# Optimization experiments

Hardware: AMD Instinct MI355X
Metric: run time of the kernel (lower is better)

## Reference

```python
import jax, jax.numpy as jnp
import numpy as np

N_NODES = 50000
NEG_SLOPE = 0.2


def gat_conv(x, src, dst, W, att_src, att_dst, bias, concat):
    # x: [N, F_in], W: [H*D, F_in], att_*: [H, D], bias: [H*D] or [D]
    N = x.shape[0]
    H, D = att_src.shape
    h = (x @ W.T).reshape(N, H, D)                      # [N, H, D]
    a_src = jnp.einsum('nhd,hd->nh', h, att_src)        # [N, H]
    a_dst = jnp.einsum('nhd,hd->nh', h, att_dst)        # [N, H]
    e = jax.nn.leaky_relu(a_src[src] + a_dst[dst], NEG_SLOPE)  # [E, H]
    # softmax over incoming edges of each destination node
    m = jax.ops.segment_max(e, dst, num_segments=N)     # [N, H]
    ex = jnp.exp(e - m[dst])
    denom = jax.ops.segment_sum(ex, dst, num_segments=N)
    alpha = ex / denom[dst]                             # [E, H]
    msg = alpha[:, :, None] * h[src]                    # [E, H, D]
    out = jax.ops.segment_sum(msg, dst, num_segments=N) # [N, H, D]
    out = out.reshape(N, H * D) if concat else out.mean(axis=1)
    return out + bias


def setup_inputs() -> dict:
    key = jax.random.key(0)
    ks = jax.random.split(key, 10)
    nfeat, nhid, nclass, heads = 256, 128, 40, 4
    d1 = nhid // heads  # 32
    E = 800000
    x = jax.random.normal(ks[0], (N_NODES, nfeat), dtype=jnp.float32)
    edge_index = jax.random.randint(ks[1], (2, E), 0, N_NODES, dtype=jnp.int64)
    s = 0.1
    W1 = jax.random.normal(ks[2], (heads * d1, nfeat), dtype=jnp.float32) * s
    att_src1 = jax.random.normal(ks[3], (heads, d1), dtype=jnp.float32) * s
    att_dst1 = jax.random.normal(ks[4], (heads, d1), dtype=jnp.float32) * s
    b1 = jnp.zeros((heads * d1,), dtype=jnp.float32)
    W2 = jax.random.normal(ks[5], (nclass, nhid), dtype=jnp.float32) * s
    att_src2 = jax.random.normal(ks[6], (1, nclass), dtype=jnp.float32) * s
    att_dst2 = jax.random.normal(ks[7], (1, nclass), dtype=jnp.float32) * s
    b2 = jnp.zeros((nclass,), dtype=jnp.float32)
    return {"x": x, "edge_index": edge_index, "W1": W1, "att_src1": att_src1,
            "att_dst1": att_dst1, "b1": b1, "W2": W2, "att_src2": att_src2,
            "att_dst2": att_dst2, "b2": b2}


def reference(x, edge_index, W1, att_src1, att_dst1, b1, W2, att_src2, att_dst2, b2):
    # PyG GATConv adds self-loops by default
    loops = jnp.arange(N_NODES, dtype=edge_index.dtype)
    src = jnp.concatenate([edge_index[0], loops])
    dst = jnp.concatenate([edge_index[1], loops])
    h = gat_conv(x, src, dst, W1, att_src1, att_dst1, b1, concat=True)
    h = jax.nn.relu(h)
    # dropout is identity in eval mode
    out = gat_conv(h, src, dst, W2, att_src2, att_dst2, b2, concat=True)
    return out
```

## Files before the change

### kernel.cpp

```cpp
#include <hip/hip_runtime.h>
#include <hip/hip_bf16.h>
#include <cstdint>
#include <cstddef>

#define N_NODES 50000
#define NEG_SLOPE 0.2f
#define NB 196
#define BIN_CHUNK 8192
#define SLICE_MAX 14336

typedef float floatx4 __attribute__((ext_vector_type(4)));
typedef short shortx8 __attribute__((ext_vector_type(8)));

__device__ __forceinline__ unsigned short f2b(float f) {
    union { float f; unsigned u; } v; v.f = f;
    unsigned u = v.u;
    return (unsigned short)((u + 0x7FFFu + ((u >> 16) & 1u)) >> 16);
}
__device__ __forceinline__ float b2f(unsigned short b) {
    union { unsigned u; float f; } v; v.u = ((unsigned)b) << 16;
    return v.f;
}

__global__ __launch_bounds__(256) void bucket_hist_kernel(
    const int* __restrict__ ei, int E0, int E, int* __restrict__ bhist,
    int* __restrict__ bhist_blk) {
    __shared__ int h[NB];
    int t = threadIdx.x;
    for (int i = t; i < NB; i += 256) h[i] = 0;
    __syncthreads();
    int base = blockIdx.x * BIN_CHUNK;
    int end = min(base + BIN_CHUNK, E);
    for (int e = base + t; e < end; e += 256) {
        int d = (e < E0) ? ei[E0 + e] : (e - E0);
        atomicAdd(&h[d >> 8], 1);
    }
    __syncthreads();
    for (int i = t; i < NB; i += 256) {
        int c = h[i];
        bhist_blk[blockIdx.x * NB + i] = c;
        if (c) atomicAdd(&bhist[i], c);
    }
}

__global__ __launch_bounds__(256) void bucket_scan_kernel(
    const int* __restrict__ bhist, int* __restrict__ bbase,
    int* __restrict__ bcursor, int* __restrict__ rowptr, int E) {
    __shared__ int buf[256];
    int t = threadIdx.x;
    int v = (t < NB) ? bhist[t] : 0;
    int x = v;
    for (int off = 1; off < 256; off <<= 1) {
        buf[t] = x; __syncthreads();
        int y = (t >= off) ? buf[t - off] : 0;
        __syncthreads();
        x += y;
    }
    if (t < NB) {
        bbase[t] = x - v;
        bcursor[t] = x - v;
    }
    if (t == NB - 1) bbase[NB] = x;
    if (t == 0) rowptr[N_NODES] = E;
}

__global__ __launch_bounds__(256) void bin_kernel(
    const int* __restrict__ ei, int E0, int E,
    int* __restrict__ bcursor, unsigned int* __restrict__ ebuf,
    const int* __restrict__ bhist_blk) {
    __shared__ int h[NB];
    __shared__ int gbase[NB];
    int t = threadIdx.x;
    for (int i = t; i < NB; i += 256) {
        int c = bhist_blk[blockIdx.x * NB + i];
        gbase[i] = c ? atomicAdd(&bcursor[i], c) : 0;
        h[i] = 0;
    }
    __syncthreads();
    int base = blockIdx.x * BIN_CHUNK;
    int end = min(base + BIN_CHUNK, E);
    for (int e = base + t; e < end; e += 256) {
        int s, d;
        if (e < E0) { s = ei[e]; d = ei[E0 + e]; }
        else        { s = e - E0; d = e - E0; }
        int b = d >> 8;
        int off = atomicAdd(&h[b], 1);
        ebuf[gbase[b] + off] = (unsigned)s | ((unsigned)(d & 255) << 16);
    }
}

__global__ __launch_bounds__(256) void build_kernel(
    const unsigned int* __restrict__ ebuf, const int* __restrict__ bbase,
    int* __restrict__ rowptr, int* __restrict__ csr_src) {
    __shared__ int h[256];
    __shared__ int lrp[257];
    __shared__ int stag[SLICE_MAX];
    int b = blockIdx.x, t = threadIdx.x;
    int e0 = bbase[b], e1 = bbase[b + 1];
    int cnt = e1 - e0;
    int n0 = b << 8;
    h[t] = 0;
    __syncthreads();
    for (int i = t; i < cnt; i += 256)
        atomicAdd(&h[ebuf[e0 + i] >> 16], 1);
    __syncthreads();
    int v = h[t], x = v;
    __shared__ int buf[256];
    for (int off = 1; off < 256; off <<= 1) {
        buf[t] = x; __syncthreads();
        int y = (t >= off) ? buf[t - off] : 0;
        __syncthreads();
        x += y;
    }
    lrp[t] = x - v;
    if (t == 255) lrp[256] = x;
    h[t] = 0;
    __syncthreads();
    int n = n0 + t;
    if (n < N_NODES) rowptr[n] = e0 + lrp[t];
    for (int i = t; i < cnt; i += 256) {
        unsigned int v2 = ebuf[e0 + i];
        int dloc = v2 >> 16;
        int off = atomicAdd(&h[dloc], 1);
        stag[lrp[dloc] + off] = (int)(v2 & 0xFFFFu);
    }
    __syncthreads();
    for (int i = t; i < cnt; i += 256) csr_src[e0 + i] = stag[i];
}

template <int BM, int BN, int NREAL, int KK, int HEADS, typename InT>
__global__ __launch_bounds__(256) void gemm_att_kernel(
    const InT* __restrict__ A, const float* __restrict__ B,
    const float* __restrict__ att_src, const float* __restrict__ att_dst,
    unsigned short* __restrict__ Cb, float* __restrict__ a_src,
    float* __restrict__ a_dst, int M) {
    const int BK = 64, LDK = 72;
    const int NT = BN / 16;
    const int MT = BM / 64;
    const int NKI = KK / BK;
    const int LDC = NREAL + 8;
    const int NAf = BM * 16 / 256;
    const int NAs = BM * 8 / 256;
    const int NBv = BN * 16 / 256;
    constexpr int SMEM = ((BM + BN) * LDK > BM * LDC) ? (BM + BN) * LDK : BM * LDC;
    __shared__ unsigned short smem[SMEM];
    unsigned short* As = smem;
    unsigned short* Bs = smem + BM * LDK;
    const int t = threadIdx.x;
    const int wave = t >> 6, lane = t & 63;
    const int lrow = lane & 15, lkg = lane >> 4;
    const int bm = blockIdx.x * BM;

    floatx4 acc[MT][NT] = {};

    float4 avf[(sizeof(InT) == 4) ? NAf : 1];
    shortx8 avs[(sizeof(InT) == 2) ? NAs : 1];
    float4 bv[NBv];

    {
        const int k0 = 0;
        if constexpr (sizeof(InT) == 4) {
#pragma unroll
            for (int q = 0; q < NAf; q++) {
                int i = t + q * 256;
                int r = i >> 4, c4 = (i & 15) << 2;
                int gr = bm + r;
                avf[q] = (gr < M) ? *(const float4*)&A[(size_t)gr * KK + k0 + c4]
                                  : make_float4(0.f, 0.f, 0.f, 0.f);
            }
        } else {
#pragma unroll
            for (int q = 0; q < NAs; q++) {
                int i = t + q * 256;
                int r = i >> 3, c8 = (i & 7) << 3;
                int gr = bm + r;
                shortx8 z = {};
                avs[q] = (gr < M) ? *(const shortx8*)&A[(size_t)gr * KK + k0 + c8] : z;
            }
        }
#pragma unroll
        for (int q = 0; q < NBv; q++) {
            int i = t + q * 256;
            int r = i >> 4, c4 = (i & 15) << 2;
            bv[q] = (r < NREAL) ? *(const float4*)&B[(size_t)r * KK + k0 + c4]
                                : make_float4(0.f, 0.f, 0.f, 0.f);
        }
    }

    for (int ki = 0; ki < NKI; ki++) {
        __syncthreads();
        if constexpr (sizeof(InT) == 4) {
#pragma unroll
            for (int q = 0; q < NAf; q++) {
                int i = t + q * 256;
                int r = i >> 4, c4 = (i & 15) << 2;
                int o = r * LDK + c4;
                float4 v = avf[q];
                As[o] = f2b(v.x); As[o + 1] = f2b(v.y);
                As[o + 2] = f2b(v.z); As[o + 3] = f2b(v.w);
            }
        } else {
#pragma unroll
            for (int q = 0; q < NAs; q++) {
                int i = t + q * 256;
                int r = i >> 3, c8 = (i & 7) << 3;
                *(shortx8*)&As[r * LDK + c8] = avs[q];
            }
        }
#pragma unroll
        for (int q = 0; q < NBv; q++) {
            int i = t + q * 256;
            int r = i >> 4, c4 = (i & 15) << 2;
            int o = r * LDK + c4;
            float4 v = bv[q];
            Bs[o] = f2b(v.x); Bs[o + 1] = f2b(v.y);
            Bs[o + 2] = f2b(v.z); Bs[o + 3] = f2b(v.w);
        }
        if (ki + 1 < NKI) {
            const int k0 = (ki + 1) * BK;
            if constexpr (sizeof(InT) == 4) {
#pragma unroll
                for (int q = 0; q < NAf; q++) {
                    int i = t + q * 256;
                    int r = i >> 4, c4 = (i & 15) << 2;
                    int gr = bm + r;
                    avf[q] = (gr < M) ? *(const float4*)&A[(size_t)gr * KK + k0 + c4]
                                      : make_float4(0.f, 0.f, 0.f, 0.f);
                }
            } else {
#pragma unroll
                for (int q = 0; q < NAs; q++) {
                    int i = t + q * 256;
                    int r = i >> 3, c8 = (i & 7) << 3;
                    int gr = bm + r;
                    shortx8 z = {};
                    avs[q] = (gr < M) ? *(const shortx8*)&A[(size_t)gr * KK + k0 + c8] : z;
                }
            }
#pragma unroll
            for (int q = 0; q < NBv; q++) {
                int i = t + q * 256;
                int r = i >> 4, c4 = (i & 15) << 2;
                bv[q] = (r < NREAL) ? *(const float4*)&B[(size_t)r * KK + k0 + c4]
                                    : make_float4(0.f, 0.f, 0.f, 0.f);
            }
        }
        __syncthreads();
        for (int ks = 0; ks < BK; ks += 32) {
            int kc = ks + lkg * 8;
#pragma unroll
            for (int mt = 0; mt < MT; mt++) {
                int row = wave * (MT * 16) + mt * 16 + lrow;
                shortx8 a = *(const shortx8*)&As[row * LDK + kc];
#pragma unroll
                for (int nt = 0; nt < NT; nt++) {
                    shortx8 b = *(const shortx8*)&Bs[(nt * 16 + lrow) * LDK + kc];
                    acc[mt][nt] = __builtin_amdgcn_mfma_f32_16x16x32_bf16(a, b, acc[mt][nt], 0, 0, 0);
                }
            }
        }
    }

    __syncthreads();
    unsigned short* Cs = smem;
#pragma unroll
    for (int mt = 0; mt < MT; mt++)
#pragma unroll
        for (int nt = 0; nt < NT; nt++)
#pragma unroll
            for (int r = 0; r < 4; r++) {
                int row = wave * (MT * 16) + mt * 16 + lkg * 4 + r;
                int col = nt * 16 + lrow;
                if (col < NREAL) Cs[row * LDC + col] = f2b(acc[mt][nt][r]);
            }
    __syncthreads();

    const int NCH = NREAL / 8;
    for (int i = t; i < BM * NCH; i += 256) {
        int row = i / NCH, ch = i - row * NCH;
        if (bm + row < M)
            *(shortx8*)&Cb[(size_t)(bm + row) * NREAL + ch * 8] =
                *(const shortx8*)&Cs[row * LDC + ch * 8];
    }

    const int D = NREAL / HEADS;
    if (t < 2 * BM) {
        int row = t >> 1, which = t & 1;
        if (bm + row < M) {
            const float* av = which ? att_dst : att_src;
            float hs[HEADS];
#pragma unroll
            for (int h = 0; h < HEADS; h++) hs[h] = 0.f;
#pragma unroll
            for (int c = 0; c < NCH; c++) {
                float4 p = *(const float4*)&av[c * 8];
                float4 q = *(const float4*)&av[c * 8 + 4];
                shortx8 cv = *(const shortx8*)&Cs[row * LDC + c * 8];
                float s = b2f((unsigned short)cv[0]) * p.x
                        + b2f((unsigned short)cv[1]) * p.y
                        + b2f((unsigned short)cv[2]) * p.z
                        + b2f((unsigned short)cv[3]) * p.w
                        + b2f((unsigned short)cv[4]) * q.x
                        + b2f((unsigned short)cv[5]) * q.y
                        + b2f((unsigned short)cv[6]) * q.z
                        + b2f((unsigned short)cv[7]) * q.w;
                hs[(c * 8) / D] += s;
            }
            float* outp = which ? a_dst : a_src;
#pragma unroll
            for (int h = 0; h < HEADS; h++)
                outp[(size_t)(bm + row) * HEADS + h] = hs[h];
        }
    }
}

__global__ __launch_bounds__(256) void agg1_kernel(
    const unsigned short* __restrict__ h1b, const float* __restrict__ a_src,
    const float* __restrict__ a_dst, const int* __restrict__ rowptr,
    const int* __restrict__ csr_src, const float* __restrict__ b1,
    unsigned short* __restrict__ zb, int N) {
    int wave = threadIdx.x >> 6, lane = threadIdx.x & 63;
    int n = blockIdx.x * 4 + wave;
    if (n >= N) return;
    int eg = lane >> 4;
    int fpos = lane & 15;
    int hd = fpos >> 2;
    int lidx = lane >> 2;
    int lh = lane & 3;
    float adn = a_dst[n * 4 + lh];
    int beg = rowptr[n], deg = rowptr[n + 1] - beg;

    float acc[8] = {0.f, 0.f, 0.f, 0.f, 0.f, 0.f, 0.f, 0.f};
    float den = 0.f;

    int s_e = (lidx < deg) ? csr_src[beg + lidx] : 0;
    float asv = a_src[(s_e << 2) + lh];

    for (int c0 = 0; c0 < deg; c0 += 16) {
        float l = asv + adn;
        l = l > 0.f ? l : NEG_SLOPE * l;
        float w_e = (c0 + lidx < deg) ? __expf(l) : 0.f;
        int cnt = min(16, deg - c0);
        int s4[4]; float w4[4]; shortx8 v4[4];
#pragma unroll
        for (int q = 0; q < 4; q++) {
            int el = (q << 2) + eg;
            s4[q] = __shfl(s_e, el << 2);
            w4[q] = __shfl(w_e, (el << 2) + hd);
        }
#pragma unroll
        for (int q = 0; q < 4; q++) {
            if (q * 4 < cnt)
                v4[q] = *(const shortx8*)&h1b[(size_t)s4[q] * 128 + fpos * 8];
        }
        int nidx = c0 + 16 + lidx;
        int s_n = (nidx < deg) ? csr_src[beg + nidx] : 0;
        float asn = a_src[(s_n << 2) + lh];
#pragma unroll
        for (int q = 0; q < 4; q++) {
            if (q * 4 < cnt) {
                float w = w4[q];
                den += w;
#pragma unroll
                for (int j = 0; j < 8; j++)
                    acc[j] += w * b2f((unsigned short)v4[q][j]);
            }
        }
        s_e = s_n; asv = asn;
    }
#pragma unroll
    for (int j = 0; j < 8; j++) {
        acc[j] += __shfl_xor(acc[j], 16);
        acc[j] += __shfl_xor(acc[j], 32);
    }
    den += __shfl_xor(den, 16);
    den += __shfl_xor(den, 32);
    if (lane < 16) {
        float inv = 1.f / den;
        float4 bb0 = *(const float4*)&b1[fpos * 8];
        float4 bb1 = *(const float4*)&b1[fpos * 8 + 4];
        shortx8 r;
        r[0] = (short)f2b(fmaxf(acc[0] * inv + bb0.x, 0.f));
        r[1] = (short)f2b(fmaxf(acc[1] * inv + bb0.y, 0.f));
        r[2] = (short)f2b(fmaxf(acc[2] * inv + bb0.z, 0.f));
        r[3] = (short)f2b(fmaxf(acc[3] * inv + bb0.w, 0.f));
        r[4] = (short)f2b(fmaxf(acc[4] * inv + bb1.x, 0.f));
        r[5] = (short)f2b(fmaxf(acc[5] * inv + bb1.y, 0.f));
        r[6] = (short)f2b(fmaxf(acc[6] * inv + bb1.z, 0.f));
        r[7] = (short)f2b(fmaxf(acc[7] * inv + bb1.w, 0.f));
        *(shortx8*)&zb[(size_t)n * 128 + fpos * 8] = r;
    }
}

__global__ __launch_bounds__(256) void agg2_kernel(
    const unsigned short* __restrict__ h2b, const float* __restrict__ a_src,
    const float* __restrict__ a_dst, const int* __restrict__ rowptr,
    const int* __restrict__ csr_src, const float* __restrict__ b2,
    float* __restrict__ out, int N) {
    int wave = threadIdx.x >> 6, lane = threadIdx.x & 63;
    int n = blockIdx.x * 4 + wave;
    if (n >= N) return;
    int eg = (lane >= 40) ? 2 : (lane >= 20 ? 1 : 0);
    int fp = lane - eg * 20;
    bool act = fp < 20;
    float adn = a_dst[n];
    int beg = rowptr[n], deg = rowptr[n + 1] - beg;

    float2 acc = {0.f, 0.f};
    float den = 0.f;
    for (int c0 = 0; c0 < deg; c0 += 48) {
        int idx = c0 + lane;
        bool cv = (lane < 48) && (idx < deg);
        int s_e = cv ? csr_src[beg + idx] : 0;
        float l = a_src[s_e] + adn;
        l = l > 0.f ? l : NEG_SLOPE * l;
        float w_e = cv ? __expf(l) : 0.f;
        int cnt = min(48, deg - c0);
#pragma unroll
        for (int qq = 0; qq < 4; qq++) {
            if (qq * 12 < cnt) {
                int s4[4]; float w4[4]; ushort2 v4[4];
#pragma unroll
                for (int q = 0; q < 4; q++) {
                    int el = qq * 12 + q * 3 + eg;
                    s4[q] = __shfl(s_e, el);
                    w4[q] = __shfl(w_e, el);
                }
#pragma unroll
                for (int q = 0; q < 4; q++) {
                    if (act)
                        v4[q] = *(const ushort2*)&h2b[(size_t)s4[q] * 40 + fp * 2];
                }
#pragma unroll
                for (int q = 0; q < 4; q++) {
                    float w = w4[q];
                    den += w;
                    if (act) {
                        acc.x += w * b2f(v4[q].x);
                        acc.y += w * b2f(v4[q].y);
                    }
                }
            }
        }
    }
    float a1x = __shfl(acc.x, fp + 20), a2x = __shfl(acc.x, fp + 40);
    float a1y = __shfl(acc.y, fp + 20), a2y = __shfl(acc.y, fp + 40);
    float d1  = __shfl(den,  fp + 20), d2  = __shfl(den,  fp + 40);
    if (lane < 20) {
        float sx = acc.x + a1x + a2x;
        float sy = acc.y + a1y + a2y;
        float dtot = den + d1 + d2;
        float inv = 1.f / dtot;
        float2 bb = *(const float2*)&b2[fp * 2];
        float2 o;
        o.x = sx * inv + bb.x;
        o.y = sy * inv + bb.y;
        *(float2*)&out[(size_t)n * 40 + fp * 2] = o;
    }
}

extern "C" void kernel_launch(void* const* d_in, const int* in_sizes, int n_in,
                              void* d_out, int out_size, void* d_ws, size_t ws_size,
                              hipStream_t stream) {
    const float* x        = (const float*)d_in[0];
    const int*   ei       = (const int*)d_in[1];
    const float* W1       = (const float*)d_in[2];
    const float* att_src1 = (const float*)d_in[3];
    const float* att_dst1 = (const float*)d_in[4];
    const float* b1       = (const float*)d_in[5];
    const float* W2       = (const float*)d_in[6];
    const float* att_src2 = (const float*)d_in[7];
    const float* att_dst2 = (const float*)d_in[8];
    const float* b2       = (const float*)d_in[9];
    float* out = (float*)d_out;

    const int N  = N_NODES;
    const int E0 = in_sizes[1] / 2;
    const int E  = E0 + N;
    const int NBLK = (E + BIN_CHUNK - 1) / BIN_CHUNK;

    char* ws = (char*)d_ws;
    unsigned short* h1b = (unsigned short*)(ws + 0);
    unsigned short* zb  = (unsigned short*)(ws + 12800000);
    unsigned short* h2b = (unsigned short*)(ws + 25600000);
    float* a_src1 = (float*)(ws + 29600000);
    float* a_dst1 = (float*)(ws + 30400000);
    float* a_src2 = (float*)(ws + 31200000);
    float* a_dst2 = (float*)(ws + 31400000);
    int*   rowptr = (int*)(ws + 31600000);
    int*   bhist  = (int*)(ws + 31800192);
    int*   bbase  = (int*)(ws + 31801088);
    int*   bcursor= (int*)(ws + 31801984);
    unsigned int* ebuf = (unsigned int*)(ws + 31802880);
    int*   csr_src= (int*)(ws + 35202880);
    int*   bhist_blk = (int*)(ws + 38602880);

    hipMemsetAsync(bhist, 0, NB * sizeof(int), stream);

    bucket_hist_kernel<<<NBLK, 256, 0, stream>>>(ei, E0, E, bhist, bhist_blk);
    bucket_scan_kernel<<<1, 256, 0, stream>>>(bhist, bbase, bcursor, rowptr, E);
    bin_kernel<<<NBLK, 256, 0, stream>>>(ei, E0, E, bcursor, ebuf, bhist_blk);
    build_kernel<<<NB, 256, 0, stream>>>(ebuf, bbase, rowptr, csr_src);

    gemm_att_kernel<128, 128, 128, 256, 4, float>
        <<<(N + 127) / 128, 256, 0, stream>>>(x, W1, att_src1, att_dst1,
                                              h1b, a_src1, a_dst1, N);
    agg1_kernel<<<(N + 3) / 4, 256, 0, stream>>>(h1b, a_src1, a_dst1, rowptr, csr_src, b1, zb, N);

    gemm_att_kernel<64, 48, 40, 128, 1, unsigned short>
        <<<(N + 63) / 64, 256, 0, stream>>>(zb, W2, att_src2, att_dst2,
                                            h2b, a_src2, a_dst2, N);
    agg2_kernel<<<(N + 3) / 4, 256, 0, stream>>>(h2b, a_src2, a_dst2, rowptr, csr_src, b2, out, N);
}
```

Measured before the change: 221.4 us.

## Fuse layer-1 GEMM with bucket histogram and last-block scan into one launch

Merges the first GEMM+attention kernel with the edge bucket-histogram kernel by giving each role its own range of block indices in one grid. The separate scan kernel is removed: the last histogram block, found through an atomic done counter, reduces the per-block histograms and writes the bucket bases. This cuts two launches and lets the GEMM and histogram work run concurrently. In exchange, the last block does a serial reduction over all per-block histograms, and the histogram blocks now reserve the GEMM's larger shared-memory allocation.

```diff
diff --git a/kernel.cpp b/kernel.cpp
--- a/kernel.cpp
+++ b/kernel.cpp
@@ -22,118 +22,13 @@
     return v.f;
 }
 
-__global__ __launch_bounds__(256) void bucket_hist_kernel(
-    const int* __restrict__ ei, int E0, int E, int* __restrict__ bhist,
-    int* __restrict__ bhist_blk) {
-    __shared__ int h[NB];
-    int t = threadIdx.x;
-    for (int i = t; i < NB; i += 256) h[i] = 0;
-    __syncthreads();
-    int base = blockIdx.x * BIN_CHUNK;
-    int end = min(base + BIN_CHUNK, E);
-    for (int e = base + t; e < end; e += 256) {
-        int d = (e < E0) ? ei[E0 + e] : (e - E0);
-        atomicAdd(&h[d >> 8], 1);
-    }
-    __syncthreads();
-    for (int i = t; i < NB; i += 256) {
-        int c = h[i];
-        bhist_blk[blockIdx.x * NB + i] = c;
-        if (c) atomicAdd(&bhist[i], c);
-    }
-}
-
-__global__ __launch_bounds__(256) void bucket_scan_kernel(
-    const int* __restrict__ bhist, int* __restrict__ bbase,
-    int* __restrict__ bcursor, int* __restrict__ rowptr, int E) {
-    __shared__ int buf[256];
-    int t = threadIdx.x;
-    int v = (t < NB) ? bhist[t] : 0;
-    int x = v;
-    for (int off = 1; off < 256; off <<= 1) {
-        buf[t] = x; __syncthreads();
-        int y = (t >= off) ? buf[t - off] : 0;
-        __syncthreads();
-        x += y;
-    }
-    if (t < NB) {
-        bbase[t] = x - v;
-        bcursor[t] = x - v;
-    }
-    if (t == NB - 1) bbase[NB] = x;
-    if (t == 0) rowptr[N_NODES] = E;
-}
-
-__global__ __launch_bounds__(256) void bin_kernel(
-    const int* __restrict__ ei, int E0, int E,
-    int* __restrict__ bcursor, unsigned int* __restrict__ ebuf,
-    const int* __restrict__ bhist_blk) {
-    __shared__ int h[NB];
-    __shared__ int gbase[NB];
-    int t = threadIdx.x;
-    for (int i = t; i < NB; i += 256) {
-        int c = bhist_blk[blockIdx.x * NB + i];
-        gbase[i] = c ? atomicAdd(&bcursor[i], c) : 0;
-        h[i] = 0;
-    }
-    __syncthreads();
-    int base = blockIdx.x * BIN_CHUNK;
-    int end = min(base + BIN_CHUNK, E);
-    for (int e = base + t; e < end; e += 256) {
-        int s, d;
-        if (e < E0) { s = ei[e]; d = ei[E0 + e]; }
-        else        { s = e - E0; d = e - E0; }
-        int b = d >> 8;
-        int off = atomicAdd(&h[b], 1);
-        ebuf[gbase[b] + off] = (unsigned)s | ((unsigned)(d & 255) << 16);
-    }
-}
-
-__global__ __launch_bounds__(256) void build_kernel(
-    const unsigned int* __restrict__ ebuf, const int* __restrict__ bbase,
-    int* __restrict__ rowptr, int* __restrict__ csr_src) {
-    __shared__ int h[256];
-    __shared__ int lrp[257];
-    __shared__ int stag[SLICE_MAX];
-    int b = blockIdx.x, t = threadIdx.x;
-    int e0 = bbase[b], e1 = bbase[b + 1];
-    int cnt = e1 - e0;
-    int n0 = b << 8;
-    h[t] = 0;
-    __syncthreads();
-    for (int i = t; i < cnt; i += 256)
-        atomicAdd(&h[ebuf[e0 + i] >> 16], 1);
-    __syncthreads();
-    int v = h[t], x = v;
-    __shared__ int buf[256];
-    for (int off = 1; off < 256; off <<= 1) {
-        buf[t] = x; __syncthreads();
-        int y = (t >= off) ? buf[t - off] : 0;
-        __syncthreads();
-        x += y;
-    }
-    lrp[t] = x - v;
-    if (t == 255) lrp[256] = x;
-    h[t] = 0;
-    __syncthreads();
-    int n = n0 + t;
-    if (n < N_NODES) rowptr[n] = e0 + lrp[t];
-    for (int i = t; i < cnt; i += 256) {
-        unsigned int v2 = ebuf[e0 + i];
-        int dloc = v2 >> 16;
-        int off = atomicAdd(&h[dloc], 1);
-        stag[lrp[dloc] + off] = (int)(v2 & 0xFFFFu);
-    }
-    __syncthreads();
-    for (int i = t; i < cnt; i += 256) csr_src[e0 + i] = stag[i];
-}
-
 template <int BM, int BN, int NREAL, int KK, int HEADS, typename InT>
-__global__ __launch_bounds__(256) void gemm_att_kernel(
+__device__ __forceinline__ void gemm_att_body(
     const InT* __restrict__ A, const float* __restrict__ B,
     const float* __restrict__ att_src, const float* __restrict__ att_dst,
     unsigned short* __restrict__ Cb, float* __restrict__ a_src,
-    float* __restrict__ a_dst, int M) {
+    float* __restrict__ a_dst, int M, int blk, int t,
+    unsigned short* smem) {
     const int BK = 64, LDK = 72;
     const int NT = BN / 16;
     const int MT = BM / 64;
@@ -142,14 +37,11 @@
     const int NAf = BM * 16 / 256;
     const int NAs = BM * 8 / 256;
     const int NBv = BN * 16 / 256;
-    constexpr int SMEM = ((BM + BN) * LDK > BM * LDC) ? (BM + BN) * LDK : BM * LDC;
-    __shared__ unsigned short smem[SMEM];
     unsigned short* As = smem;
     unsigned short* Bs = smem + BM * LDK;
-    const int t = threadIdx.x;
     const int wave = t >> 6, lane = t & 63;
     const int lrow = lane & 15, lkg = lane >> 4;
-    const int bm = blockIdx.x * BM;
+    const int bm = blk * BM;
 
     floatx4 acc[MT][NT] = {};
 
@@ -312,6 +204,140 @@
                 outp[(size_t)(bm + row) * HEADS + h] = hs[h];
         }
     }
+}
+
+template <int BM, int BN, int NREAL, int KK, int HEADS, typename InT>
+__global__ __launch_bounds__(256) void gemm_att_kernel(
+    const InT* __restrict__ A, const float* __restrict__ B,
+    const float* __restrict__ att_src, const float* __restrict__ att_dst,
+    unsigned short* __restrict__ Cb, float* __restrict__ a_src,
+    float* __restrict__ a_dst, int M) {
+    constexpr int SMEM = ((BM + BN) * 72 > BM * (NREAL + 8)) ? (BM + BN) * 72
+                                                             : BM * (NREAL + 8);
+    __shared__ unsigned short smem[SMEM];
+    gemm_att_body<BM, BN, NREAL, KK, HEADS, InT>(
+        A, B, att_src, att_dst, Cb, a_src, a_dst, M,
+        blockIdx.x, threadIdx.x, smem);
+}
+
+__global__ __launch_bounds__(256) void fused_gemm1_hist_kernel(
+    const float* __restrict__ x, const float* __restrict__ W1,
+    const float* __restrict__ att_src, const float* __restrict__ att_dst,
+    unsigned short* __restrict__ h1b, float* __restrict__ a_src,
+    float* __restrict__ a_dst, int M, int G_GEMM,
+    const int* __restrict__ ei, int E0, int E, int nblk,
+    int* __restrict__ bhist_blk, int* __restrict__ done,
+    int* __restrict__ bbase, int* __restrict__ bcursor,
+    int* __restrict__ rowptr) {
+    __shared__ unsigned short smem[(128 + 128) * 72];
+    int t = threadIdx.x;
+    if ((int)blockIdx.x < G_GEMM) {
+        gemm_att_body<128, 128, 128, 256, 4, float>(
+            x, W1, att_src, att_dst, h1b, a_src, a_dst, M,
+            blockIdx.x, t, smem);
+        return;
+    }
+    int hb = blockIdx.x - G_GEMM;
+    int* h   = (int*)smem;
+    int* buf = h + 256;
+    for (int i = t; i < NB; i += 256) h[i] = 0;
+    __syncthreads();
+    int base = hb * BIN_CHUNK;
+    int end = min(base + BIN_CHUNK, E);
+    for (int e = base + t; e < end; e += 256) {
+        int d = (e < E0) ? ei[E0 + e] : (e - E0);
+        atomicAdd(&h[d >> 8], 1);
+    }
+    __syncthreads();
+    for (int i = t; i < NB; i += 256)
+        bhist_blk[hb * NB + i] = h[i];
+    __threadfence();
+    __shared__ int lastFlag;
+    if (t == 0) lastFlag = (atomicAdd(done, 1) == nblk - 1) ? 1 : 0;
+    __syncthreads();
+    if (!lastFlag) return;
+    __threadfence();
+    int v = 0;
+    if (t < NB)
+        for (int blk = 0; blk < nblk; blk++)
+            v += bhist_blk[blk * NB + t];
+    int xacc = v;
+    for (int off = 1; off < 256; off <<= 1) {
+        buf[t] = xacc; __syncthreads();
+        int y = (t >= off) ? buf[t - off] : 0;
+        __syncthreads();
+        xacc += y;
+    }
+    if (t < NB) {
+        bbase[t] = xacc - v;
+        bcursor[t] = xacc - v;
+    }
+    if (t == NB - 1) bbase[NB] = xacc;
+    if (t == 0) rowptr[N_NODES] = E;
+}
+
+__global__ __launch_bounds__(256) void bin_kernel(
+    const int* __restrict__ ei, int E0, int E,
+    int* __restrict__ bcursor, unsigned int* __restrict__ ebuf,
+    const int* __restrict__ bhist_blk) {
+    __shared__ int h[NB];
+    __shared__ int gbase[NB];
+    int t = threadIdx.x;
+    for (int i = t; i < NB; i += 256) {
+        int c = bhist_blk[blockIdx.x * NB + i];
+        gbase[i] = c ? atomicAdd(&bcursor[i], c) : 0;
+        h[i] = 0;
+    }
+    __syncthreads();
+    int base = blockIdx.x * BIN_CHUNK;
+    int end = min(base + BIN_CHUNK, E);
+    for (int e = base + t; e < end; e += 256) {
+        int s, d;
+        if (e < E0) { s = ei[e]; d = ei[E0 + e]; }
+        else        { s = e - E0; d = e - E0; }
+        int b = d >> 8;
+        int off = atomicAdd(&h[b], 1);
+        ebuf[gbase[b] + off] = (unsigned)s | ((unsigned)(d & 255) << 16);
+    }
+}
+
+__global__ __launch_bounds__(256) void build_kernel(
+    const unsigned int* __restrict__ ebuf, const int* __restrict__ bbase,
+    int* __restrict__ rowptr, int* __restrict__ csr_src) {
+    __shared__ int h[256];
+    __shared__ int lrp[257];
+    __shared__ int stag[SLICE_MAX];
+    int b = blockIdx.x, t = threadIdx.x;
+    int e0 = bbase[b], e1 = bbase[b + 1];
+    int cnt = e1 - e0;
+    int n0 = b << 8;
+    h[t] = 0;
+    __syncthreads();
+    for (int i = t; i < cnt; i += 256)
+        atomicAdd(&h[ebuf[e0 + i] >> 16], 1);
+    __syncthreads();
+    int v = h[t], x = v;
+    __shared__ int buf[256];
+    for (int off = 1; off < 256; off <<= 1) {
+        buf[t] = x; __syncthreads();
+        int y = (t >= off) ? buf[t - off] : 0;
+        __syncthreads();
+        x += y;
+    }
+    lrp[t] = x - v;
+    if (t == 255) lrp[256] = x;
+    h[t] = 0;
+    __syncthreads();
+    int n = n0 + t;
+    if (n < N_NODES) rowptr[n] = e0 + lrp[t];
+    for (int i = t; i < cnt; i += 256) {
+        unsigned int v2 = ebuf[e0 + i];
+        int dloc = v2 >> 16;
+        int off = atomicAdd(&h[dloc], 1);
+        stag[lrp[dloc] + off] = (int)(v2 & 0xFFFFu);
+    }
+    __syncthreads();
+    for (int i = t; i < cnt; i += 256) csr_src[e0 + i] = stag[i];
 }
 
 __global__ __launch_bounds__(256) void agg1_kernel(
@@ -478,6 +504,7 @@
     const int E0 = in_sizes[1] / 2;
     const int E  = E0 + N;
     const int NBLK = (E + BIN_CHUNK - 1) / BIN_CHUNK;
+    const int G_GEMM = (N + 127) / 128;
 
     char* ws = (char*)d_ws;
     unsigned short* h1b = (unsigned short*)(ws + 0);
@@ -488,23 +515,21 @@
     float* a_src2 = (float*)(ws + 31200000);
     float* a_dst2 = (float*)(ws + 31400000);
     int*   rowptr = (int*)(ws + 31600000);
-    int*   bhist  = (int*)(ws + 31800192);
+    int*   done   = (int*)(ws + 31800192);
     int*   bbase  = (int*)(ws + 31801088);
     int*   bcursor= (int*)(ws + 31801984);
     unsigned int* ebuf = (unsigned int*)(ws + 31802880);
     int*   csr_src= (int*)(ws + 35202880);
     int*   bhist_blk = (int*)(ws + 38602880);
 
-    hipMemsetAsync(bhist, 0, NB * sizeof(int), stream);
-
-    bucket_hist_kernel<<<NBLK, 256, 0, stream>>>(ei, E0, E, bhist, bhist_blk);
-    bucket_scan_kernel<<<1, 256, 0, stream>>>(bhist, bbase, bcursor, rowptr, E);
+    hipMemsetAsync(done, 0, sizeof(int), stream);
+
+    fused_gemm1_hist_kernel<<<G_GEMM + NBLK, 256, 0, stream>>>(
+        x, W1, att_src1, att_dst1, h1b, a_src1, a_dst1, N, G_GEMM,
+        ei, E0, E, NBLK, bhist_blk, done, bbase, bcursor, rowptr);
     bin_kernel<<<NBLK, 256, 0, stream>>>(ei, E0, E, bcursor, ebuf, bhist_blk);
     build_kernel<<<NB, 256, 0, stream>>>(ebuf, bbase, rowptr, csr_src);
 
-    gemm_att_kernel<128, 128, 128, 256, 4, float>
-        <<<(N + 127) / 128, 256, 0, stream>>>(x, W1, att_src1, att_dst1,
-                                              h1b, a_src1, a_dst1, N);
     agg1_kernel<<<(N + 3) / 4, 256, 0, stream>>>(h1b, a_src1, a_dst1, rowptr, csr_src, b1, zb, N);
 
     gemm_att_kernel<64, 48, 40, 128, 1, unsigned short>
```

After: 229.4 us. 3.6% more time.

## Add dedicated layer-1 GEMM kernel loading A directly into registers

Applied to the files above, without the earlier changes.

Replaces the generic templated GEMM for the first layer with a specialised kernel. It uses 64-row tiles, stages W1 in LDS in two 128-wide K halves, and reads x rows straight from global memory into MFMA A-fragments, converting to bf16 in registers so A never goes through shared memory. The generic template loses its fp32-input path. The aim is to halve LDS traffic and conversion overhead for the 256-wide fp32 input and to launch more blocks, at the cost of less coalesced direct row loads and reloading W1 per block.

```diff
diff --git a/kernel.cpp b/kernel.cpp
--- a/kernel.cpp
+++ b/kernel.cpp
@@ -128,6 +128,114 @@
     for (int i = t; i < cnt; i += 256) csr_src[e0 + i] = stag[i];
 }
 
+#define G1_LDB 132
+__global__ __launch_bounds__(256) void gemm1_att_kernel(
+    const float* __restrict__ A, const float* __restrict__ B,
+    const float* __restrict__ att_src, const float* __restrict__ att_dst,
+    unsigned short* __restrict__ Cb, float* __restrict__ a_src,
+    float* __restrict__ a_dst, int M) {
+    __shared__ unsigned short smem[128 * G1_LDB];
+    const int t = threadIdx.x;
+    const int wave = t >> 6, lane = t & 63;
+    const int lrow = lane & 15, lkg = lane >> 4;
+    const int bm = blockIdx.x * 64;
+    const int grow = bm + wave * 16 + lrow;
+    const float* arow = A + (size_t)grow * 256;
+    const bool rowok = grow < M;
+
+    floatx4 acc[8] = {};
+
+    for (int h = 0; h < 2; h++) {
+        const int kbase = h * 128;
+        if (h) __syncthreads();
+#pragma unroll
+        for (int q = 0; q < 16; q++) {
+            int i = t + q * 256;
+            int r = i >> 5, c4 = (i & 31) << 2;
+            float4 v = *(const float4*)&B[(size_t)r * 256 + kbase + c4];
+            ushort4 w;
+            w.x = f2b(v.x); w.y = f2b(v.y); w.z = f2b(v.z); w.w = f2b(v.w);
+            *(ushort4*)&smem[r * G1_LDB + c4] = w;
+        }
+        __syncthreads();
+        float4 av0[2], av1[2], av2[2], av3[2];
+        if (rowok) {
+            int k0 = kbase + lkg * 8;
+            av0[0] = *(const float4*)&arow[k0];      av0[1] = *(const float4*)&arow[k0 + 4];
+            av1[0] = *(const float4*)&arow[k0 + 32]; av1[1] = *(const float4*)&arow[k0 + 36];
+            av2[0] = *(const float4*)&arow[k0 + 64]; av2[1] = *(const float4*)&arow[k0 + 68];
+            av3[0] = *(const float4*)&arow[k0 + 96]; av3[1] = *(const float4*)&arow[k0 + 100];
+        } else {
+            av0[0]=av0[1]=av1[0]=av1[1]=av2[0]=av2[1]=av3[0]=av3[1]=make_float4(0.f,0.f,0.f,0.f);
+        }
+#pragma unroll
+        for (int s = 0; s < 4; s++) {
+            float4 lo = (s==0)?av0[0]:(s==1)?av1[0]:(s==2)?av2[0]:av3[0];
+            float4 hi = (s==0)?av0[1]:(s==1)?av1[1]:(s==2)?av2[1]:av3[1];
+            shortx8 a;
+            a[0]=(short)f2b(lo.x); a[1]=(short)f2b(lo.y);
+            a[2]=(short)f2b(lo.z); a[3]=(short)f2b(lo.w);
+            a[4]=(short)f2b(hi.x); a[5]=(short)f2b(hi.y);
+            a[6]=(short)f2b(hi.z); a[7]=(short)f2b(hi.w);
+            int kloc = s * 32 + lkg * 8;
+#pragma unroll
+            for (int nt = 0; nt < 8; nt++) {
+                shortx8 b = *(const shortx8*)&smem[(nt * 16 + lrow) * G1_LDB + kloc];
+                acc[nt] = __builtin_amdgcn_mfma_f32_16x16x32_bf16(a, b, acc[nt], 0, 0, 0);
+            }
+        }
+    }
+
+    __syncthreads();
+    const int LDC = 136;
+    unsigned short* Cs = smem;
+#pragma unroll
+    for (int nt = 0; nt < 8; nt++)
+#pragma unroll
+        for (int r = 0; r < 4; r++) {
+            int row = wave * 16 + lkg * 4 + r;
+            int col = nt * 16 + lrow;
+            Cs[row * LDC + col] = f2b(acc[nt][r]);
+        }
+    __syncthreads();
+
+#pragma unroll
+    for (int q = 0; q < 4; q++) {
+        int i = t + q * 256;
+        int row = i >> 4, ch = i & 15;
+        if (bm + row < M)
+            *(shortx8*)&Cb[(size_t)(bm + row) * 128 + ch * 8] =
+                *(const shortx8*)&Cs[row * LDC + ch * 8];
+    }
+
+    if (t < 128) {
+        int row = t >> 1, which = t & 1;
+        if (bm + row < M) {
+            const float* av = which ? att_dst : att_src;
+            float hs[4] = {0.f, 0.f, 0.f, 0.f};
+#pragma unroll
+            for (int c = 0; c < 16; c++) {
+                float4 p = *(const float4*)&av[c * 8];
+                float4 q2 = *(const float4*)&av[c * 8 + 4];
+                shortx8 cv = *(const shortx8*)&Cs[row * LDC + c * 8];
+                float s = b2f((unsigned short)cv[0]) * p.x
+                        + b2f((unsigned short)cv[1]) * p.y
+                        + b2f((unsigned short)cv[2]) * p.z
+                        + b2f((unsigned short)cv[3]) * p.w
+                        + b2f((unsigned short)cv[4]) * q2.x
+                        + b2f((unsigned short)cv[5]) * q2.y
+                        + b2f((unsigned short)cv[6]) * q2.z
+                        + b2f((unsigned short)cv[7]) * q2.w;
+                hs[c >> 2] += s;
+            }
+            float* outp = which ? a_dst : a_src;
+#pragma unroll
+            for (int hh = 0; hh < 4; hh++)
+                outp[(size_t)(bm + row) * 4 + hh] = hs[hh];
+        }
+    }
+}
+
 template <int BM, int BN, int NREAL, int KK, int HEADS, typename InT>
 __global__ __launch_bounds__(256) void gemm_att_kernel(
     const InT* __restrict__ A, const float* __restrict__ B,
@@ -139,10 +247,10 @@
     const int MT = BM / 64;
     const int NKI = KK / BK;
     const int LDC = NREAL + 8;
-    const int NAf = BM * 16 / 256;
     const int NAs = BM * 8 / 256;
     const int NBv = BN * 16 / 256;
-    constexpr int SMEM = ((BM + BN) * LDK > BM * LDC) ? (BM + BN) * LDK : BM * LDC;
+    constexpr int SMEM = ((BM + BN) * 72 > BM * (NREAL + 8)) ? (BM + BN) * 72
+                                                             : BM * (NREAL + 8);
     __shared__ unsigned short smem[SMEM];
     unsigned short* As = smem;
     unsigned short* Bs = smem + BM * LDK;
@@ -152,31 +260,18 @@
     const int bm = blockIdx.x * BM;
 
     floatx4 acc[MT][NT] = {};
-
-    float4 avf[(sizeof(InT) == 4) ? NAf : 1];
-    shortx8 avs[(sizeof(InT) == 2) ? NAs : 1];
+    shortx8 avs[NAs];
     float4 bv[NBv];
 
     {
         const int k0 = 0;
-        if constexpr (sizeof(InT) == 4) {
-#pragma unroll
-            for (int q = 0; q < NAf; q++) {
-                int i = t + q * 256;
-                int r = i >> 4, c4 = (i & 15) << 2;
-                int gr = bm + r;
-                avf[q] = (gr < M) ? *(const float4*)&A[(size_t)gr * KK + k0 + c4]
-                                  : make_float4(0.f, 0.f, 0.f, 0.f);
-            }
-        } else {
-#pragma unroll
-            for (int q = 0; q < NAs; q++) {
-                int i = t + q * 256;
-                int r = i >> 3, c8 = (i & 7) << 3;
-                int gr = bm + r;
-                shortx8 z = {};
-                avs[q] = (gr < M) ? *(const shortx8*)&A[(size_t)gr * KK + k0 + c8] : z;
-            }
+#pragma unroll
+        for (int q = 0; q < NAs; q++) {
+            int i = t + q * 256;
+            int r = i >> 3, c8 = (i & 7) << 3;
+            int gr = bm + r;
+            shortx8 z = {};
+            avs[q] = (gr < M) ? *(const shortx8*)&A[(size_t)gr * KK + k0 + c8] : z;
         }
 #pragma unroll
         for (int q = 0; q < NBv; q++) {
@@ -189,23 +284,11 @@
 
     for (int ki = 0; ki < NKI; ki++) {
         __syncthreads();
-        if constexpr (sizeof(InT) == 4) {
-#pragma unroll
-            for (int q = 0; q < NAf; q++) {
-                int i = t + q * 256;
-                int r = i >> 4, c4 = (i & 15) << 2;
-                int o = r * LDK + c4;
-                float4 v = avf[q];
-                As[o] = f2b(v.x); As[o + 1] = f2b(v.y);
-                As[o + 2] = f2b(v.z); As[o + 3] = f2b(v.w);
-            }
-        } else {
-#pragma unroll
-            for (int q = 0; q < NAs; q++) {
-                int i = t + q * 256;
-                int r = i >> 3, c8 = (i & 7) << 3;
-                *(shortx8*)&As[r * LDK + c8] = avs[q];
-            }
+#pragma unroll
+        for (int q = 0; q < NAs; q++) {
+            int i = t + q * 256;
+            int r = i >> 3, c8 = (i & 7) << 3;
+            *(shortx8*)&As[r * LDK + c8] = avs[q];
         }
 #pragma unroll
         for (int q = 0; q < NBv; q++) {
@@ -218,24 +301,13 @@
         }
         if (ki + 1 < NKI) {
             const int k0 = (ki + 1) * BK;
-            if constexpr (sizeof(InT) == 4) {
-#pragma unroll
-                for (int q = 0; q < NAf; q++) {
-                    int i = t + q * 256;
-                    int r = i >> 4, c4 = (i & 15) << 2;
-                    int gr = bm + r;
-                    avf[q] = (gr < M) ? *(const float4*)&A[(size_t)gr * KK + k0 + c4]
-                                      : make_float4(0.f, 0.f, 0.f, 0.f);
-                }
-            } else {
-#pragma unroll
-                for (int q = 0; q < NAs; q++) {
-                    int i = t + q * 256;
-                    int r = i >> 3, c8 = (i & 7) << 3;
-                    int gr = bm + r;
-                    shortx8 z = {};
-                    avs[q] = (gr < M) ? *(const shortx8*)&A[(size_t)gr * KK + k0 + c8] : z;
-                }
+#pragma unroll
+            for (int q = 0; q < NAs; q++) {
+                int i = t + q * 256;
+                int r = i >> 3, c8 = (i & 7) << 3;
+                int gr = bm + r;
+                shortx8 z = {};
+                avs[q] = (gr < M) ? *(const shortx8*)&A[(size_t)gr * KK + k0 + c8] : z;
             }
 #pragma unroll
             for (int q = 0; q < NBv; q++) {
@@ -502,9 +574,8 @@
     bin_kernel<<<NBLK, 256, 0, stream>>>(ei, E0, E, bcursor, ebuf, bhist_blk);
     build_kernel<<<NB, 256, 0, stream>>>(ebuf, bbase, rowptr, csr_src);
 
-    gemm_att_kernel<128, 128, 128, 256, 4, float>
-        <<<(N + 127) / 128, 256, 0, stream>>>(x, W1, att_src1, att_dst1,
-                                              h1b, a_src1, a_dst1, N);
+    gemm1_att_kernel<<<(N + 63) / 64, 256, 0, stream>>>(
+        x, W1, att_src1, att_dst1, h1b, a_src1, a_dst1, N);
     agg1_kernel<<<(N + 3) / 4, 256, 0, stream>>>(h1b, a_src1, a_dst1, rowptr, csr_src, b1, zb, N);
 
     gemm_att_kernel<64, 48, 40, 128, 1, unsigned short>
```

New measurement: 222.6 us. No clear change (+0.5%).
